# Optimization experiments

Measured on AMD Instinct MI355X. Metric: run time of the kernel, lower is better.

## Reference

```python
import jax, jax.numpy as jnp
import numpy as np
from jax import lax

EPS = 1e-12  # tf.nn.l2_normalize epsilon


def setup_inputs() -> dict:
    key = jax.random.key(0)
    k1, k2, k3 = jax.random.split(key, 3)
    B, T, D, C, F, K = 64, 2048, 1024, 1024, 256, 5
    sentence_embed = jax.random.normal(k1, (B, T, D), dtype=jnp.float32)
    label_embed = jax.random.normal(k2, (C, D), dtype=jnp.float32)
    conv_w = jax.random.normal(k3, (K, C, F), dtype=jnp.float32) * 0.05
    conv_b = jnp.zeros((F,), dtype=jnp.float32)
    return {"sentence_embed": sentence_embed, "label_embed": label_embed,
            "conv_w": conv_w, "conv_b": conv_b}


def reference(sentence_embed, label_embed, conv_w, conv_b):
    # l2-normalize label embeddings along feature dim (tf.nn.l2_normalize semantics)
    sq = jnp.sum(label_embed * label_embed, axis=-1, keepdims=True)
    label_norm = label_embed * lax.rsqrt(jnp.maximum(sq, EPS))
    # G: [B, T, C] = sentence_embed @ label_norm^T (raw sentence_embed, per original)
    G = jnp.einsum('btd,cd->btc', sentence_embed, label_norm)
    # Conv1D over time, 'same' padding, relu: [B, T, F]
    conv = lax.conv_general_dilated(
        G, conv_w, window_strides=(1,), padding='SAME',
        dimension_numbers=('NWC', 'WIO', 'NWC'))
    conv = jax.nn.relu(conv + conv_b)
    # max over filters -> attention values [B, T] (NOT softmaxed in original output path)
    att_v = jnp.max(conv, axis=-1)
    # batch_dot(sentence_embed, att_v, axes=[1,1]) -> [B, D]
    H_enc = jnp.einsum('btd,bt->bd', sentence_embed, att_v)
    return H_enc
```

## Files before the change

kernel.cpp:

```cpp
#include <hip/hip_runtime.h>

typedef unsigned short u16;
typedef __attribute__((ext_vector_type(4))) float f32x4;
typedef __attribute__((ext_vector_type(8))) short s16x8;
typedef __attribute__((ext_vector_type(4))) unsigned short u16x4;

#define DEV __device__ __forceinline__

constexpr int Bb = 64, Tt = 2048, Dd = 1024, Cc = 1024, Ff = 256;
constexpr int TP = Tt + 4;
constexpr int M1 = Bb * Tt;

DEV u16 f2bf(float f) {
    union { float f; unsigned u; } v; v.f = f;
    unsigned r = v.u + 0x7fffu + ((v.u >> 16) & 1u);
    return (u16)(r >> 16);
}
DEV float bf2f(u16 h) {
    union { unsigned u; float f; } v; v.u = ((unsigned)h) << 16; return v.f;
}

DEV void gl_lds16(const u16* g, u16* l) {
    __builtin_amdgcn_global_load_lds(
        (const __attribute__((address_space(1))) unsigned*)(const void*)g,
        (__attribute__((address_space(3))) unsigned*)(void*)l,
        16, 0, 0);
}

DEV int swz_scol(int lane) { return (((lane & 7) ^ ((lane >> 3) & 7)) << 3); }
DEV int swz_rd(int row, int e) { return e ^ ((row & 7) << 3); }

__global__ __launch_bounds__(256) void k_s2bf(const float* __restrict__ S,
                                              u16* __restrict__ Sb) {
    size_t i = ((size_t)blockIdx.x * 256 + threadIdx.x) * 8;
    const size_t stride = (size_t)gridDim.x * 256 * 8;
    const size_t n = (size_t)M1 * Dd;
    for (; i < n; i += stride) {
        f32x4 a = *(const f32x4*)(S + i);
        f32x4 b = *(const f32x4*)(S + i + 4);
        s16x8 r;
        r[0] = (short)f2bf(a.x); r[1] = (short)f2bf(a.y);
        r[2] = (short)f2bf(a.z); r[3] = (short)f2bf(a.w);
        r[4] = (short)f2bf(b.x); r[5] = (short)f2bf(b.y);
        r[6] = (short)f2bf(b.z); r[7] = (short)f2bf(b.w);
        *(s16x8*)(Sb + i) = r;
    }
}

__global__ __launch_bounds__(256) void k_label_norm(const float* __restrict__ L,
                                                    u16* __restrict__ Ln) {
    int c = blockIdx.x;
    int t = threadIdx.x;
    const float* row = L + (size_t)c * Dd;
    float s = 0.f;
    for (int d = t; d < Dd; d += 256) { float v = row[d]; s += v * v; }
    for (int o = 32; o; o >>= 1) s += __shfl_down(s, o);
    __shared__ float red[4];
    if ((t & 63) == 0) red[t >> 6] = s;
    __syncthreads();
    float tot = red[0] + red[1] + red[2] + red[3];
    float r = rsqrtf(fmaxf(tot, 1e-12f));
    for (int d = t; d < Dd; d += 256) Ln[(size_t)c * Dd + d] = f2bf(row[d] * r);
}

__global__ __launch_bounds__(256) void k_wt(const float* __restrict__ W,
                                            u16* __restrict__ Wt) {
    __shared__ float tile[64][65];
    int k = blockIdx.x; int c0 = blockIdx.y * 64; int f0 = blockIdx.z * 64;
    int tid = threadIdx.x;
    const float* Wk = W + (size_t)k * Cc * Ff;
    #pragma unroll
    for (int i = 0; i < 16; ++i) {
        int q = tid + i * 256;
        int ci = q >> 6, fj = q & 63;
        tile[ci][fj] = Wk[(size_t)(c0 + ci) * Ff + f0 + fj];
    }
    __syncthreads();
    #pragma unroll
    for (int i = 0; i < 16; ++i) {
        int q = tid + i * 256;
        int fi = q >> 6, cj = q & 63;
        Wt[((size_t)k * Ff + f0 + fi) * Cc + c0 + cj] = f2bf(tile[cj][fi]);
    }
}

__global__ __launch_bounds__(256) void k_zpad(u16* __restrict__ Gp) {
    int b_ = blockIdx.x, tid = threadIdx.x;
    size_t base = (size_t)b_ * TP * Cc;
    for (int i = tid; i < 2 * Cc; i += 256) {
        Gp[base + i] = 0;
        Gp[base + (size_t)(TP - 2) * Cc + i] = 0;
    }
}

__global__ __launch_bounds__(256) void k_gemm1_bf(const u16* __restrict__ Sb,
                                                  const u16* __restrict__ Ln,
                                                  u16* __restrict__ Gp) {
    __shared__ alignas(16) u16 As[128 * 64];
    __shared__ alignas(16) u16 Bs[128 * 64];
    int bid = blockIdx.x;
    int xcd = bid & 7, idx = bid >> 3;
    int mt = xcd * 128 + (idx >> 3);
    int nt = idx & 7;
    const int m0 = mt * 128, n0 = nt * 128;
    int tid = threadIdx.x;
    int lane = tid & 63, wid = tid >> 6;
    int wm = wid >> 1, wn = wid & 1;
    int srow = lane >> 3;
    int scol = swz_scol(lane);
    f32x4 acc[4][4] = {};

    for (int kt = 0; kt < 16; ++kt) {
        int k0 = kt * 64;
        #pragma unroll
        for (int i = 0; i < 4; ++i) {
            int seg = wid * 4 + i;
            int r0 = seg * 8;
            gl_lds16(Sb + (size_t)(m0 + r0 + srow) * Dd + k0 + scol, &As[seg * 512]);
            gl_lds16(Ln + (size_t)(n0 + r0 + srow) * Dd + k0 + scol, &Bs[seg * 512]);
        }
        __syncthreads();
        #pragma unroll
        for (int kk = 0; kk < 2; ++kk) {
            int rsel = lane & 15, ksel = kk * 32 + (lane >> 4) * 8;
            s16x8 a[4], b[4];
            #pragma unroll
            for (int f = 0; f < 4; ++f) {
                int row = wm * 64 + f * 16 + rsel;
                a[f] = *(const s16x8*)&As[row * 64 + swz_rd(row, ksel)];
            }
            #pragma unroll
            for (int f = 0; f < 4; ++f) {
                int row = wn * 64 + f * 16 + rsel;
                b[f] = *(const s16x8*)&Bs[row * 64 + swz_rd(row, ksel)];
            }
            #pragma unroll
            for (int fm = 0; fm < 4; ++fm)
                #pragma unroll
                for (int fn = 0; fn < 4; ++fn)
                    acc[fm][fn] = __builtin_amdgcn_mfma_f32_16x16x32_bf16(
                        a[fm], b[fn], acc[fm][fn], 0, 0, 0);
        }
        __syncthreads();
    }
    #pragma unroll
    for (int fm = 0; fm < 4; ++fm) {
        #pragma unroll
        for (int r = 0; r < 4; ++r) {
            int row = m0 + wm * 64 + fm * 16 + (lane >> 4) * 4 + r;
            int b_ = row >> 11, t = row & 2047;
            size_t base = ((size_t)b_ * TP + t + 2) * Cc;
            #pragma unroll
            for (int fn = 0; fn < 4; ++fn) {
                int col = n0 + wn * 64 + fn * 16 + (lane & 15);
                Gp[base + col] = f2bf(acc[fm][fn][r]);
            }
        }
    }
}

__global__ __launch_bounds__(256) void k_gemm1_f32(const float* __restrict__ S,
                                                   const u16* __restrict__ Ln,
                                                   u16* __restrict__ Gp) {
    __shared__ alignas(16) u16 As[128 * 64];
    __shared__ alignas(16) u16 Bs[128 * 64];
    int bid = blockIdx.x;
    int xcd = bid & 7, idx = bid >> 3;
    int mt = xcd * 128 + (idx >> 3);
    int nt = idx & 7;
    const int m0 = mt * 128, n0 = nt * 128;
    int tid = threadIdx.x;
    int lane = tid & 63, wid = tid >> 6;
    int wm = wid >> 1, wn = wid & 1;
    f32x4 acc[4][4] = {};

    for (int kt = 0; kt < 16; ++kt) {
        int k0 = kt * 64;
        #pragma unroll
        for (int i = 0; i < 8; ++i) {
            int q = tid + i * 256;
            int row = q >> 4, c4 = (q & 15) * 4;
            f32x4 v = *(const f32x4*)(S + (size_t)(m0 + row) * Dd + k0 + c4);
            u16* p = &As[row * 64 + c4];
            p[0] = f2bf(v.x); p[1] = f2bf(v.y); p[2] = f2bf(v.z); p[3] = f2bf(v.w);
        }
        #pragma unroll
        for (int i = 0; i < 4; ++i) {
            int q = tid + i * 256;
            int row = q >> 3, c8 = (q & 7) * 8;
            *(s16x8*)&Bs[row * 64 + c8] =
                *(const s16x8*)(Ln + (size_t)(n0 + row) * Dd + k0 + c8);
        }
        __syncthreads();
        #pragma unroll
        for (int kk = 0; kk < 2; ++kk) {
            int rsel = lane & 15, ksel = kk * 32 + (lane >> 4) * 8;
            s16x8 a[4], b[4];
            #pragma unroll
            for (int f = 0; f < 4; ++f)
                a[f] = *(const s16x8*)&As[(wm * 64 + f * 16 + rsel) * 64 + ksel];
            #pragma unroll
            for (int f = 0; f < 4; ++f)
                b[f] = *(const s16x8*)&Bs[(wn * 64 + f * 16 + rsel) * 64 + ksel];
            #pragma unroll
            for (int fm = 0; fm < 4; ++fm)
                #pragma unroll
                for (int fn = 0; fn < 4; ++fn)
                    acc[fm][fn] = __builtin_amdgcn_mfma_f32_16x16x32_bf16(
                        a[fm], b[fn], acc[fm][fn], 0, 0, 0);
        }
        __syncthreads();
    }
    #pragma unroll
    for (int fm = 0; fm < 4; ++fm) {
        #pragma unroll
        for (int r = 0; r < 4; ++r) {
            int row = m0 + wm * 64 + fm * 16 + (lane >> 4) * 4 + r;
            int b_ = row >> 11, t = row & 2047;
            size_t base = ((size_t)b_ * TP + t + 2) * Cc;
            #pragma unroll
            for (int fn = 0; fn < 4; ++fn) {
                int col = n0 + wn * 64 + fn * 16 + (lane & 15);
                Gp[base + col] = f2bf(acc[fm][fn][r]);
            }
        }
    }
}

__global__ __launch_bounds__(512) void k_conv(const u16* __restrict__ Gp,
                                              const u16* __restrict__ Wt,
                                              const float* __restrict__ bias,
                                              float* __restrict__ att) {
    __shared__ alignas(16) u16 As[136 * 64];
    __shared__ alignas(16) u16 Bs[256 * 64];
    __shared__ float red[4][128];
    int mt = blockIdx.x;
    int b_ = mt >> 4;
    int t0 = (mt & 15) * 128;
    int tid = threadIdx.x, lane = tid & 63, wid = tid >> 6;
    int wm = wid >> 2, wn = wid & 3;
    int srow = lane >> 3, scol = swz_scol(lane);
    f32x4 acc[4][4] = {};
    const size_t gbase = ((size_t)b_ * TP + t0) * Cc;

    for (int ct = 0; ct < 16; ++ct) {
        int c0 = ct * 64;
        for (int s = wid; s < 17; s += 8)
            gl_lds16(Gp + gbase + (size_t)(s * 8 + srow) * Cc + c0 + scol, &As[s * 512]);
        for (int k = 0; k < 5; ++k) {
            #pragma unroll
            for (int i = 0; i < 4; ++i) {
                int seg = wid * 4 + i;
                gl_lds16(Wt + ((size_t)k * Ff + seg * 8 + srow) * Cc + c0 + scol,
                         &Bs[seg * 512]);
            }
            __syncthreads();
            #pragma unroll
            for (int kk = 0; kk < 2; ++kk) {
                int rsel = lane & 15, ksel = kk * 32 + (lane >> 4) * 8;
                s16x8 a[4], b[4];
                #pragma unroll
                for (int f = 0; f < 4; ++f) {
                    int row = k + wm * 64 + f * 16 + rsel;
                    a[f] = *(const s16x8*)&As[row * 64 + swz_rd(row, ksel)];
                }
                #pragma unroll
                for (int f = 0; f < 4; ++f) {
                    int row = wn * 64 + f * 16 + rsel;
                    b[f] = *(const s16x8*)&Bs[row * 64 + swz_rd(row, ksel)];
                }
                #pragma unroll
                for (int fm = 0; fm < 4; ++fm)
                    #pragma unroll
                    for (int fn = 0; fn < 4; ++fn)
                        acc[fm][fn] = __builtin_amdgcn_mfma_f32_16x16x32_bf16(
                            a[fm], b[fn], acc[fm][fn], 0, 0, 0);
            }
            __syncthreads();
        }
    }
    float bv[4];
    #pragma unroll
    for (int fn = 0; fn < 4; ++fn)
        bv[fn] = bias[wn * 64 + fn * 16 + (lane & 15)];
    #pragma unroll
    for (int fm = 0; fm < 4; ++fm) {
        #pragma unroll
        for (int r = 0; r < 4; ++r) {
            float v = 0.f;
            #pragma unroll
            for (int fn = 0; fn < 4; ++fn)
                v = fmaxf(v, fmaxf(acc[fm][fn][r] + bv[fn], 0.f));
            #pragma unroll
            for (int m = 1; m <= 8; m <<= 1) v = fmaxf(v, __shfl_xor(v, m));
            if ((lane & 15) == 0)
                red[wn][wm * 64 + fm * 16 + (lane >> 4) * 4 + r] = v;
        }
    }
    __syncthreads();
    if (tid < 128) {
        float v = fmaxf(fmaxf(red[0][tid], red[1][tid]),
                        fmaxf(red[2][tid], red[3][tid]));
        att[(size_t)mt * 128 + tid] = v;
    }
}

__global__ __launch_bounds__(256) void k_henc_bf(const u16* __restrict__ Sb,
                                                 const float* __restrict__ att,
                                                 float* __restrict__ part) {
    int b_ = blockIdx.x, tc = blockIdx.y;
    int tid = threadIdx.x;
    int d = tid * 4;
    const u16* Sp = Sb + ((size_t)b_ * Tt + (size_t)tc * 256) * Dd + d;
    const float* ap = att + (size_t)b_ * Tt + (size_t)tc * 256;
    f32x4 acc = {};
    for (int t = 0; t < 256; ++t) {
        float a = ap[t];
        u16x4 s = *(const u16x4*)(Sp + (size_t)t * Dd);
        acc.x += bf2f(s.x) * a;
        acc.y += bf2f(s.y) * a;
        acc.z += bf2f(s.z) * a;
        acc.w += bf2f(s.w) * a;
    }
    *(f32x4*)(part + ((size_t)tc * Bb + b_) * Dd + d) = acc;
}

__global__ __launch_bounds__(256) void k_henc_f32(const float* __restrict__ S,
                                                  const float* __restrict__ att,
                                                  float* __restrict__ part) {
    int b_ = blockIdx.x, tc = blockIdx.y;
    int tid = threadIdx.x;
    int d = tid * 4;
    const float* Sp = S + ((size_t)b_ * Tt + (size_t)tc * 256) * Dd + d;
    const float* ap = att + (size_t)b_ * Tt + (size_t)tc * 256;
    f32x4 acc = {};
    for (int t = 0; t < 256; ++t) {
        float a = ap[t];
        f32x4 s = *(const f32x4*)(Sp + (size_t)t * Dd);
        acc += s * a;
    }
    *(f32x4*)(part + ((size_t)tc * Bb + b_) * Dd + d) = acc;
}

__global__ __launch_bounds__(256) void k_hred(const float* __restrict__ part,
                                              float* __restrict__ out) {
    int i = blockIdx.x * 256 + threadIdx.x;
    float s = 0.f;
    #pragma unroll
    for (int p = 0; p < 8; ++p) s += part[(size_t)p * (Bb * Dd) + i];
    out[i] = s;
}

extern "C" void kernel_launch(void* const* d_in, const int* in_sizes, int n_in,
                              void* d_out, int out_size, void* d_ws, size_t ws_size,
                              hipStream_t stream) {
    const float* S  = (const float*)d_in[0];
    const float* L  = (const float*)d_in[1];
    const float* W  = (const float*)d_in[2];
    const float* cb = (const float*)d_in[3];
    float* out = (float*)d_out;
    char* ws = (char*)d_ws;

    const size_t GP_B   = (size_t)Bb * TP * Cc * 2;
    const size_t LN_B   = (size_t)Cc * Dd * 2;
    const size_t WT_B   = (size_t)5 * Ff * Cc * 2;
    const size_t ATT_B  = (size_t)M1 * 4;
    const size_t PART_B = (size_t)8 * Bb * Dd * 4;
    const size_t SB_B   = (size_t)M1 * Dd * 2;
    u16*   Gp   = (u16*)(ws);
    u16*   Ln   = (u16*)(ws + GP_B);
    u16*   Wt   = (u16*)(ws + GP_B + LN_B);
    float* att  = (float*)(ws + GP_B + LN_B + WT_B);
    float* part = (float*)(ws + GP_B + LN_B + WT_B + ATT_B);
    u16*   Sb   = (u16*)(ws + GP_B + LN_B + WT_B + ATT_B + PART_B);
    const bool use_bf = ws_size >= GP_B + LN_B + WT_B + ATT_B + PART_B + SB_B;

    k_label_norm<<<Cc, 256, 0, stream>>>(L, Ln);
    k_wt<<<dim3(5, Cc / 64, Ff / 64), 256, 0, stream>>>(W, Wt);
    k_zpad<<<Bb, 256, 0, stream>>>(Gp);
    if (use_bf) {
        k_s2bf<<<2048, 256, 0, stream>>>(S, Sb);
        k_gemm1_bf<<<(M1 / 128) * (Cc / 128), 256, 0, stream>>>(Sb, Ln, Gp);
    } else {
        k_gemm1_f32<<<(M1 / 128) * (Cc / 128), 256, 0, stream>>>(S, Ln, Gp);
    }
    k_conv<<<M1 / 128, 512, 0, stream>>>(Gp, Wt, cb, att);
    if (use_bf) k_henc_bf<<<dim3(Bb, 8), 256, 0, stream>>>(Sb, att, part);
    else        k_henc_f32<<<dim3(Bb, 8), 256, 0, stream>>>(S, att, part);
    k_hred<<<(Bb * Dd) / 256, 256, 0, stream>>>(part, out);
}
```

Baseline: 946.5 us.

## Double-buffer conv kernel LDS loads and enlarge time tile to 256

The conv kernel now double-buffers both the G tile and the weight tile in LDS, issuing the next stage's global-to-LDS loads before computing the current one, so memory latency overlaps MFMA work. The time tile doubles from 128 to 256 rows per block, and each wave now covers 64x128 outputs with 32 accumulators. This cuts redundant weight reloads and halo overhead per block. In exchange it uses more LDS and registers, and the launch grid is halved to 512 blocks, which may limit occupancy.

```diff
diff --git a/kernel.cpp b/kernel.cpp
--- a/kernel.cpp
+++ b/kernel.cpp
@@ -227,69 +227,84 @@
     }
 }
 
-__global__ __launch_bounds__(512) void k_conv(const u16* __restrict__ Gp,
-                                              const u16* __restrict__ Wt,
-                                              const float* __restrict__ bias,
-                                              float* __restrict__ att) {
-    __shared__ alignas(16) u16 As[136 * 64];
-    __shared__ alignas(16) u16 Bs[256 * 64];
-    __shared__ float red[4][128];
+__global__ __launch_bounds__(512, 2) void k_conv(const u16* __restrict__ Gp,
+                                                 const u16* __restrict__ Wt,
+                                                 const float* __restrict__ bias,
+                                                 float* __restrict__ att) {
+    __shared__ alignas(16) u16 As[2][33 * 512];
+    __shared__ alignas(16) u16 Bs[2][256 * 64];
+    __shared__ float red[2][256];
     int mt = blockIdx.x;
-    int b_ = mt >> 4;
-    int t0 = (mt & 15) * 128;
+    int b_ = mt >> 3;
+    int t0 = (mt & 7) * 256;
     int tid = threadIdx.x, lane = tid & 63, wid = tid >> 6;
-    int wm = wid >> 2, wn = wid & 3;
+    int wm = wid >> 1, wn = wid & 1;
     int srow = lane >> 3, scol = swz_scol(lane);
-    f32x4 acc[4][4] = {};
+    f32x4 acc[4][8] = {};
     const size_t gbase = ((size_t)b_ * TP + t0) * Cc;
 
+    auto STAGE_B = [&](int ct, int k, int buf) {
+        int c0 = ct * 64;
+        #pragma unroll
+        for (int i = 0; i < 4; ++i) {
+            int seg = wid * 4 + i;
+            gl_lds16(Wt + ((size_t)k * Ff + seg * 8 + srow) * Cc + c0 + scol,
+                     &Bs[buf][seg * 512]);
+        }
+    };
+    auto STAGE_A = [&](int ct, int buf) {
+        int c0 = ct * 64;
+        for (int s = wid; s < 33; s += 8)
+            gl_lds16(Gp + gbase + (size_t)(s * 8 + srow) * Cc + c0 + scol,
+                     &As[buf][s * 512]);
+    };
+
+    STAGE_A(0, 0);
+    STAGE_B(0, 0, 0);
+    __syncthreads();
+
+    int ca = 0, cb = 0;
     for (int ct = 0; ct < 16; ++ct) {
-        int c0 = ct * 64;
-        for (int s = wid; s < 17; s += 8)
-            gl_lds16(Gp + gbase + (size_t)(s * 8 + srow) * Cc + c0 + scol, &As[s * 512]);
         for (int k = 0; k < 5; ++k) {
-            #pragma unroll
-            for (int i = 0; i < 4; ++i) {
-                int seg = wid * 4 + i;
-                gl_lds16(Wt + ((size_t)k * Ff + seg * 8 + srow) * Cc + c0 + scol,
-                         &Bs[seg * 512]);
-            }
-            __syncthreads();
+            if (k < 4)       STAGE_B(ct, k + 1, cb ^ 1);
+            else if (ct < 15) { STAGE_B(ct + 1, 0, cb ^ 1); STAGE_A(ct + 1, ca ^ 1); }
             #pragma unroll
             for (int kk = 0; kk < 2; ++kk) {
                 int rsel = lane & 15, ksel = kk * 32 + (lane >> 4) * 8;
-                s16x8 a[4], b[4];
+                s16x8 a[4], b[8];
                 #pragma unroll
                 for (int f = 0; f < 4; ++f) {
                     int row = k + wm * 64 + f * 16 + rsel;
-                    a[f] = *(const s16x8*)&As[row * 64 + swz_rd(row, ksel)];
+                    a[f] = *(const s16x8*)&As[ca][row * 64 + swz_rd(row, ksel)];
                 }
                 #pragma unroll
-                for (int f = 0; f < 4; ++f) {
-                    int row = wn * 64 + f * 16 + rsel;
-                    b[f] = *(const s16x8*)&Bs[row * 64 + swz_rd(row, ksel)];
+                for (int f = 0; f < 8; ++f) {
+                    int row = wn * 128 + f * 16 + rsel;
+                    b[f] = *(const s16x8*)&Bs[cb][row * 64 + swz_rd(row, ksel)];
                 }
                 #pragma unroll
                 for (int fm = 0; fm < 4; ++fm)
                     #pragma unroll
-                    for (int fn = 0; fn < 4; ++fn)
+                    for (int fn = 0; fn < 8; ++fn)
                         acc[fm][fn] = __builtin_amdgcn_mfma_f32_16x16x32_bf16(
                             a[fm], b[fn], acc[fm][fn], 0, 0, 0);
             }
             __syncthreads();
-        }
-    }
-    float bv[4];
-    #pragma unroll
-    for (int fn = 0; fn < 4; ++fn)
-        bv[fn] = bias[wn * 64 + fn * 16 + (lane & 15)];
+            cb ^= 1;
+            if (k == 4) ca ^= 1;
+        }
+    }
+    float bv[8];
+    #pragma unroll
+    for (int fn = 0; fn < 8; ++fn)
+        bv[fn] = bias[wn * 128 + fn * 16 + (lane & 15)];
     #pragma unroll
     for (int fm = 0; fm < 4; ++fm) {
         #pragma unroll
         for (int r = 0; r < 4; ++r) {
             float v = 0.f;
             #pragma unroll
-            for (int fn = 0; fn < 4; ++fn)
+            for (int fn = 0; fn < 8; ++fn)
                 v = fmaxf(v, fmaxf(acc[fm][fn][r] + bv[fn], 0.f));
             #pragma unroll
             for (int m = 1; m <= 8; m <<= 1) v = fmaxf(v, __shfl_xor(v, m));
@@ -298,11 +313,8 @@
         }
     }
     __syncthreads();
-    if (tid < 128) {
-        float v = fmaxf(fmaxf(red[0][tid], red[1][tid]),
-                        fmaxf(red[2][tid], red[3][tid]));
-        att[(size_t)mt * 128 + tid] = v;
-    }
+    if (tid < 256)
+        att[(size_t)mt * 256 + tid] = fmaxf(red[0][tid], red[1][tid]);
 }
 
 __global__ __launch_bounds__(256) void k_henc_bf(const u16* __restrict__ Sb,
@@ -384,7 +396,7 @@
     } else {
         k_gemm1_f32<<<(M1 / 128) * (Cc / 128), 256, 0, stream>>>(S, Ln, Gp);
     }
-    k_conv<<<M1 / 128, 512, 0, stream>>>(Gp, Wt, cb, att);
+    k_conv<<<M1 / 256, 512, 0, stream>>>(Gp, Wt, cb, att);
     if (use_bf) k_henc_bf<<<dim3(Bb, 8), 256, 0, stream>>>(Sb, att, part);
     else        k_henc_f32<<<dim3(Bb, 8), 256, 0, stream>>>(S, att, part);
     k_hred<<<(Bb * Dd) / 256, 256, 0, stream>>>(part, out);
```

Result: no change. 964.2 us (+1.9%).

## Rewrite bf16 GEMM1 as 256x256 double-buffered 8-wave pipelined kernel

Applied to the files above, without the earlier changes.

Replaces the 128x128 single-buffered bf16 GEMM for G with a 256x256 tile, 512-thread kernel that double-buffers LDS and stages the next K tile in halves interleaved between MFMA phases. It uses s_setprio around the MFMA blocks and raw barriers to overlap global-to-LDS loads with compute. The larger tile raises data reuse. The cost is heavier register pressure (32 accumulators per thread) and 128KB of LDS per block, which may limit occupancy.

```diff
diff --git a/kernel.cpp b/kernel.cpp
--- a/kernel.cpp
+++ b/kernel.cpp
@@ -93,67 +93,135 @@
     }
 }
 
-__global__ __launch_bounds__(256) void k_gemm1_bf(const u16* __restrict__ Sb,
-                                                  const u16* __restrict__ Ln,
-                                                  u16* __restrict__ Gp) {
-    __shared__ alignas(16) u16 As[128 * 64];
-    __shared__ alignas(16) u16 Bs[128 * 64];
+__global__ __launch_bounds__(512, 2) void k_gemm1_8ph(const u16* __restrict__ Sb,
+                                                      const u16* __restrict__ Ln,
+                                                      u16* __restrict__ Gp) {
+    __shared__ alignas(16) u16 As[2][256 * 64];
+    __shared__ alignas(16) u16 Bs[2][256 * 64];
     int bid = blockIdx.x;
     int xcd = bid & 7, idx = bid >> 3;
-    int mt = xcd * 128 + (idx >> 3);
-    int nt = idx & 7;
-    const int m0 = mt * 128, n0 = nt * 128;
-    int tid = threadIdx.x;
-    int lane = tid & 63, wid = tid >> 6;
-    int wm = wid >> 1, wn = wid & 1;
-    int srow = lane >> 3;
-    int scol = swz_scol(lane);
-    f32x4 acc[4][4] = {};
+    int mt = xcd * 64 + (idx >> 2);
+    int nt = idx & 3;
+    const int m0 = mt * 256, n0 = nt * 256;
+    int tid = threadIdx.x, lane = tid & 63, wid = tid >> 6;
+    int wm = wid >> 2, wn = wid & 3;
+    int srow = lane >> 3, scol = swz_scol(lane);
+    const int rsel = lane & 15;
+    const int klo = (lane >> 4) * 8, khi = 32 + klo;
+    f32x4 acc[8][4] = {};
+
+    auto stageA = [&](int kt, int h, int buf) {
+        #pragma unroll
+        for (int i = 0; i < 2; ++i) {
+            int seg = h * 16 + wid * 2 + i;
+            gl_lds16(Sb + (size_t)(m0 + seg * 8 + srow) * Dd + kt * 64 + scol,
+                     &As[buf][seg * 512]);
+        }
+    };
+    auto stageB = [&](int kt, int h, int buf) {
+        #pragma unroll
+        for (int i = 0; i < 2; ++i) {
+            int seg = h * 16 + wid * 2 + i;
+            gl_lds16(Ln + (size_t)(n0 + seg * 8 + srow) * Dd + kt * 64 + scol,
+                     &Bs[buf][seg * 512]);
+        }
+    };
+
+    stageA(0, 0, 0); stageA(0, 1, 0);
+    stageB(0, 0, 0); stageB(0, 1, 0);
+    asm volatile("s_waitcnt vmcnt(0)" ::: "memory");
+    asm volatile("s_barrier" ::: "memory");
 
     for (int kt = 0; kt < 16; ++kt) {
-        int k0 = kt * 64;
-        #pragma unroll
-        for (int i = 0; i < 4; ++i) {
-            int seg = wid * 4 + i;
-            int r0 = seg * 8;
-            gl_lds16(Sb + (size_t)(m0 + r0 + srow) * Dd + k0 + scol, &As[seg * 512]);
-            gl_lds16(Ln + (size_t)(n0 + r0 + srow) * Dd + k0 + scol, &Bs[seg * 512]);
-        }
-        __syncthreads();
-        #pragma unroll
-        for (int kk = 0; kk < 2; ++kk) {
-            int rsel = lane & 15, ksel = kk * 32 + (lane >> 4) * 8;
-            s16x8 a[4], b[4];
-            #pragma unroll
-            for (int f = 0; f < 4; ++f) {
-                int row = wm * 64 + f * 16 + rsel;
-                a[f] = *(const s16x8*)&As[row * 64 + swz_rd(row, ksel)];
-            }
-            #pragma unroll
-            for (int f = 0; f < 4; ++f) {
-                int row = wn * 64 + f * 16 + rsel;
-                b[f] = *(const s16x8*)&Bs[row * 64 + swz_rd(row, ksel)];
-            }
-            #pragma unroll
-            for (int fm = 0; fm < 4; ++fm)
-                #pragma unroll
-                for (int fn = 0; fn < 4; ++fn)
-                    acc[fm][fn] = __builtin_amdgcn_mfma_f32_16x16x32_bf16(
-                        a[fm], b[fn], acc[fm][fn], 0, 0, 0);
-        }
-        __syncthreads();
-    }
-    #pragma unroll
-    for (int fm = 0; fm < 4; ++fm) {
+        const int cur = kt & 1, nxt = cur ^ 1;
+        const u16* Ab = As[cur];
+        const u16* Bq = Bs[cur];
+        s16x8 a[4], b[4];
+        #pragma unroll
+        for (int f = 0; f < 4; ++f) {
+            int row = wm * 128 + f * 16 + rsel;
+            a[f] = *(const s16x8*)&Ab[row * 64 + swz_rd(row, klo)];
+        }
+        #pragma unroll
+        for (int f = 0; f < 4; ++f) {
+            int row = wn * 64 + f * 16 + rsel;
+            b[f] = *(const s16x8*)&Bq[row * 64 + swz_rd(row, klo)];
+        }
+        if (kt < 15) { stageA(kt + 1, 0, nxt); stageB(kt + 1, 0, nxt); }
+        __builtin_amdgcn_s_barrier();
+        __builtin_amdgcn_s_setprio(1);
+        #pragma unroll
+        for (int fm = 0; fm < 4; ++fm)
+            #pragma unroll
+            for (int fn = 0; fn < 4; ++fn)
+                acc[fm][fn] = __builtin_amdgcn_mfma_f32_16x16x32_bf16(
+                    a[fm], b[fn], acc[fm][fn], 0, 0, 0);
+        __builtin_amdgcn_s_setprio(0);
+        __builtin_amdgcn_s_barrier();
+        #pragma unroll
+        for (int f = 0; f < 4; ++f) {
+            int row = wm * 128 + 64 + f * 16 + rsel;
+            a[f] = *(const s16x8*)&Ab[row * 64 + swz_rd(row, klo)];
+        }
+        if (kt < 15) { stageA(kt + 1, 1, nxt); stageB(kt + 1, 1, nxt); }
+        __builtin_amdgcn_s_barrier();
+        __builtin_amdgcn_s_setprio(1);
+        #pragma unroll
+        for (int fm = 0; fm < 4; ++fm)
+            #pragma unroll
+            for (int fn = 0; fn < 4; ++fn)
+                acc[4 + fm][fn] = __builtin_amdgcn_mfma_f32_16x16x32_bf16(
+                    a[fm], b[fn], acc[4 + fm][fn], 0, 0, 0);
+        __builtin_amdgcn_s_setprio(0);
+        __builtin_amdgcn_s_barrier();
+        #pragma unroll
+        for (int f = 0; f < 4; ++f) {
+            int row = wm * 128 + f * 16 + rsel;
+            a[f] = *(const s16x8*)&Ab[row * 64 + swz_rd(row, khi)];
+        }
+        #pragma unroll
+        for (int f = 0; f < 4; ++f) {
+            int row = wn * 64 + f * 16 + rsel;
+            b[f] = *(const s16x8*)&Bq[row * 64 + swz_rd(row, khi)];
+        }
+        __builtin_amdgcn_s_barrier();
+        __builtin_amdgcn_s_setprio(1);
+        #pragma unroll
+        for (int fm = 0; fm < 4; ++fm)
+            #pragma unroll
+            for (int fn = 0; fn < 4; ++fn)
+                acc[fm][fn] = __builtin_amdgcn_mfma_f32_16x16x32_bf16(
+                    a[fm], b[fn], acc[fm][fn], 0, 0, 0);
+        __builtin_amdgcn_s_setprio(0);
+        __builtin_amdgcn_s_barrier();
+        #pragma unroll
+        for (int f = 0; f < 4; ++f) {
+            int row = wm * 128 + 64 + f * 16 + rsel;
+            a[f] = *(const s16x8*)&Ab[row * 64 + swz_rd(row, khi)];
+        }
+        __builtin_amdgcn_s_barrier();
+        __builtin_amdgcn_s_setprio(1);
+        #pragma unroll
+        for (int fm = 0; fm < 4; ++fm)
+            #pragma unroll
+            for (int fn = 0; fn < 4; ++fn)
+                acc[4 + fm][fn] = __builtin_amdgcn_mfma_f32_16x16x32_bf16(
+                    a[fm], b[fn], acc[4 + fm][fn], 0, 0, 0);
+        __builtin_amdgcn_s_setprio(0);
+        asm volatile("s_waitcnt vmcnt(0)" ::: "memory");
+        asm volatile("s_barrier" ::: "memory");
+    }
+    #pragma unroll
+    for (int m = 0; m < 8; ++m) {
         #pragma unroll
         for (int r = 0; r < 4; ++r) {
-            int row = m0 + wm * 64 + fm * 16 + (lane >> 4) * 4 + r;
+            int row = m0 + wm * 128 + (m >> 2) * 64 + (m & 3) * 16 + (lane >> 4) * 4 + r;
             int b_ = row >> 11, t = row & 2047;
             size_t base = ((size_t)b_ * TP + t + 2) * Cc;
             #pragma unroll
-            for (int fn = 0; fn < 4; ++fn) {
-                int col = n0 + wn * 64 + fn * 16 + (lane & 15);
-                Gp[base + col] = f2bf(acc[fm][fn][r]);
+            for (int n = 0; n < 4; ++n) {
+                int col = n0 + wn * 64 + n * 16 + rsel;
+                Gp[base + col] = f2bf(acc[m][n][r]);
             }
         }
     }
@@ -380,7 +448,7 @@
     k_zpad<<<Bb, 256, 0, stream>>>(Gp);
     if (use_bf) {
         k_s2bf<<<2048, 256, 0, stream>>>(S, Sb);
-        k_gemm1_bf<<<(M1 / 128) * (Cc / 128), 256, 0, stream>>>(Sb, Ln, Gp);
+        k_gemm1_8ph<<<(M1 / 256) * (Cc / 256), 512, 0, stream>>>(Sb, Ln, Gp);
     } else {
         k_gemm1_f32<<<(M1 / 128) * (Cc / 128), 256, 0, stream>>>(S, Ln, Gp);
     }
```

Result: no change. 958.5 us (+1.3%).
